# Optimization experiments

Hardware: AMD Instinct MI355X
Metric: run time of the kernel (lower is better)

Reference implementation:

```python
import jax, jax.numpy as jnp
import numpy as np

N = 100000
D_FEAT = 256
HID = 128
EMB = 64
FANOUT = 16


def setup_inputs() -> dict:
    key = jax.random.key(0)
    k = jax.random.split(key, 7)
    s = 0.05
    features = jax.random.normal(k[0], (N, D_FEAT), dtype=jnp.float32)
    W1 = jax.random.normal(k[1], (HID, 2 * D_FEAT), dtype=jnp.float32) * s
    W2 = jax.random.normal(k[2], (HID, 2 * HID), dtype=jnp.float32) * s
    W3 = jax.random.normal(k[3], (HID, 2 * HID), dtype=jnp.float32) * s
    W4 = jax.random.normal(k[4], (EMB, 2 * HID), dtype=jnp.float32) * s
    nodes = jnp.arange(N, dtype=jnp.int32)
    neigh = jax.random.randint(k[5], (N, FANOUT), 0, N, dtype=jnp.int32)
    return {"features": features, "W1": W1, "W2": W2, "W3": W3, "W4": W4,
            "nodes": nodes, "neigh": neigh}


def _sage_layer(h, neigh, W):
    # MeanAggregator: mean of sampled neighbor features  [N, d]
    neigh_mean = jnp.mean(h[neigh], axis=1)
    # Encoder (gcn=False): relu(W @ cat([self, neigh_mean]).T) -> [N, out]
    combined = jnp.concatenate([h, neigh_mean], axis=1)  # [N, 2d]
    return jax.nn.relu(combined @ W.T)


def reference(features, W1, W2, W3, W4, nodes, neigh):
    h1 = _sage_layer(features, neigh, W1)  # [N, HID]
    h2 = _sage_layer(h1, neigh, W2)        # [N, HID]
    h3 = _sage_layer(h2, neigh, W3)        # [N, HID]
    h4 = _sage_layer(h3, neigh, W4)        # [N, EMB]
    # GraphEmbeddingModule.forward returns gSAGE4(n).t() -> [len(n), EMB]
    return h4[nodes]
```

## Files before the change

### kernel.cpp

```cpp
#include <hip/hip_runtime.h>
#include <hip/hip_bf16.h>


constexpr int N_NODES = 100000;
constexpr int FANOUT  = 16;

typedef __attribute__((ext_vector_type(8))) short short8;
typedef __attribute__((ext_vector_type(4))) float f32x4;

__device__ inline unsigned short bf16_rne(float f) {
    unsigned u = __float_as_uint(f);
    return (unsigned short)((u + 0x7fffu + ((u >> 16) & 1u)) >> 16);
}
__device__ inline float bf16_tof(unsigned short s) {
    return __uint_as_float(((unsigned)s) << 16);
}

__global__ __launch_bounds__(256)
void prep_Bsw(const float* __restrict__ W, unsigned short* __restrict__ Bhi,
              unsigned short* __restrict__ Blo, int D_IN, int D_OUT)
{
    int i = blockIdx.x * 256 + threadIdx.x;
    int total = 2 * D_OUT * D_IN;
    if (i >= total) return;
    int K = D_IN, C = 2 * D_OUT;
    int c = i / K, k = i % K;
    float v = (c < D_OUT) ? W[(size_t)c * (2 * K) + k]
                          : W[(size_t)(c - D_OUT) * (2 * K) + K + k];
    int tc = c >> 4, mlc = c & 15;
    int tk = k >> 5, qk = (k >> 3) & 3, e = k & 7;
    size_t off = ((size_t)(tk * (C / 16) + tc) * 64 + qk * 16 + mlc) * 8 + e;
    unsigned short hi = bf16_rne(v);
    Bhi[off] = hi;
    Blo[off] = bf16_rne(v - bf16_tof(hi));
}

__global__ __launch_bounds__(256, 6)
void gemm1(const float* __restrict__ hf,
           const unsigned short* __restrict__ Bhi,
           const unsigned short* __restrict__ Blo,
           float* __restrict__ gs, unsigned short* __restrict__ gn, int N)
{
    constexpr int K = 256, DO = 128, LDA = 40;
    __shared__ unsigned short Ah[32 * LDA], Al[32 * LDA];

    const int tid  = threadIdx.x;
    const int wave = tid >> 6;
    const int lane = tid & 63;
    const int ml   = lane & 15;
    const int quad = lane >> 4;
    const int node0 = blockIdx.x * 32;

    const int srow = tid >> 3;
    const int sc4  = tid & 7;
    int nd = node0 + srow; if (nd >= N) nd = N - 1;
    const float* pA = &hf[(size_t)nd * K + sc4 * 4];

    f32x4 acc[2][4];
    #pragma unroll
    for (int mi = 0; mi < 2; ++mi)
        #pragma unroll
        for (int ni = 0; ni < 4; ++ni)
            acc[mi][ni] = (f32x4){0.f, 0.f, 0.f, 0.f};

    float4 pf = *(const float4*)&pA[0];

    for (int k0 = 0; k0 < K; k0 += 32) {
        {
            float vv[4] = {pf.x, pf.y, pf.z, pf.w};
            unsigned short hi[4], lo[4];
            #pragma unroll
            for (int e = 0; e < 4; ++e) {
                hi[e] = bf16_rne(vv[e]);
                lo[e] = bf16_rne(vv[e] - bf16_tof(hi[e]));
            }
            *(uint2*)&Ah[srow * LDA + sc4 * 4] = *(const uint2*)hi;
            *(uint2*)&Al[srow * LDA + sc4 * 4] = *(const uint2*)lo;
        }
        if (k0 + 32 < K) pf = *(const float4*)&pA[k0 + 32];
        __syncthreads();

        short8 afh[2], afl[2];
        #pragma unroll
        for (int mi = 0; mi < 2; ++mi) {
            int r = mi * 16 + ml;
            afh[mi] = *(const short8*)&Ah[r * LDA + quad * 8];
            afl[mi] = *(const short8*)&Al[r * LDA + quad * 8];
        }
        const size_t bbase = (size_t)((k0 >> 5) * 16 + wave * 4) * 512 + (size_t)lane * 8;
        #pragma unroll
        for (int ni = 0; ni < 4; ++ni) {
            short8 bh = *(const short8*)&Bhi[bbase + ni * 512];
            short8 bl = *(const short8*)&Blo[bbase + ni * 512];
            #pragma unroll
            for (int mi = 0; mi < 2; ++mi) {
                acc[mi][ni] = __builtin_amdgcn_mfma_f32_16x16x32_bf16(afl[mi], bh, acc[mi][ni], 0, 0, 0);
                acc[mi][ni] = __builtin_amdgcn_mfma_f32_16x16x32_bf16(afh[mi], bl, acc[mi][ni], 0, 0, 0);
                acc[mi][ni] = __builtin_amdgcn_mfma_f32_16x16x32_bf16(afh[mi], bh, acc[mi][ni], 0, 0, 0);
            }
        }
        __syncthreads();
    }

    #pragma unroll
    for (int mi = 0; mi < 2; ++mi)
        #pragma unroll
        for (int r = 0; r < 4; ++r) {
            int node = node0 + mi * 16 + quad * 4 + r;
            if (node >= N) continue;
            #pragma unroll
            for (int ni = 0; ni < 4; ++ni) {
                int c = wave * 64 + ni * 16 + ml;
                float v = acc[mi][ni][r];
                if (c < DO) gs[(size_t)node * DO + c] = v;
                else        gn[(size_t)node * DO + (c - DO)] = bf16_rne(v);
            }
        }
}

template<int C>
__global__ __launch_bounds__(256, 8)
void fused_layer(const float* __restrict__ gs_in,
                 const unsigned short* __restrict__ gn_in,
                 const int* __restrict__ neigh,
                 const unsigned short* __restrict__ Bhi,
                 const unsigned short* __restrict__ Blo,
                 float* __restrict__ gs_out,
                 unsigned short* __restrict__ gn_out, int N)
{
    constexpr int K = 128, DO = C / 2, NI = C / 64;
    __shared__ unsigned short Afh[32 * 128], Afl[32 * 128];

    const int tid  = threadIdx.x;
    const int wave = tid >> 6;
    const int lane = tid & 63;
    const int ml   = lane & 15;
    const int quad = lane >> 4;
    const int node0 = blockIdx.x * 32;

    {
        const int row = tid >> 3;
        const int s   = tid & 7;
        const int c0  = 64 * (s >> 2) + 8 * (s & 3);
        const int c1  = c0 + 32;
        int nd = node0 + row; if (nd >= N) nd = N - 1;
        const int4* nb4 = (const int4*)(neigh + (size_t)nd * FANOUT);
        int4 q0 = nb4[0], q1 = nb4[1], q2 = nb4[2], q3 = nb4[3];
        int ids[FANOUT] = {q0.x, q0.y, q0.z, q0.w, q1.x, q1.y, q1.z, q1.w,
                           q2.x, q2.y, q2.z, q2.w, q3.x, q3.y, q3.z, q3.w};
        float acc[16];
        #pragma unroll
        for (int c = 0; c < 16; ++c) acc[c] = 0.f;
        #pragma unroll
        for (int j = 0; j < FANOUT; ++j) {
            const uint4* src = (const uint4*)&gn_in[(size_t)ids[j] * 128];
            uint4 qa = src[c0 >> 3];
            uint4 qb = src[c1 >> 3];
            acc[0]  += __uint_as_float(qa.x << 16);
            acc[1]  += __uint_as_float(qa.x & 0xffff0000u);
            acc[2]  += __uint_as_float(qa.y << 16);
            acc[3]  += __uint_as_float(qa.y & 0xffff0000u);
            acc[4]  += __uint_as_float(qa.z << 16);
            acc[5]  += __uint_as_float(qa.z & 0xffff0000u);
            acc[6]  += __uint_as_float(qa.w << 16);
            acc[7]  += __uint_as_float(qa.w & 0xffff0000u);
            acc[8]  += __uint_as_float(qb.x << 16);
            acc[9]  += __uint_as_float(qb.x & 0xffff0000u);
            acc[10] += __uint_as_float(qb.y << 16);
            acc[11] += __uint_as_float(qb.y & 0xffff0000u);
            acc[12] += __uint_as_float(qb.z << 16);
            acc[13] += __uint_as_float(qb.z & 0xffff0000u);
            acc[14] += __uint_as_float(qb.w << 16);
            acc[15] += __uint_as_float(qb.w & 0xffff0000u);
        }
        const float inv = 1.0f / (float)FANOUT;
        const float* gsp = &gs_in[(size_t)nd * 128];
        #pragma unroll
        for (int cc = 0; cc < 2; ++cc) {
            const int ch = cc ? c1 : c0;
            float4 g0 = *(const float4*)&gsp[ch];
            float4 g1 = *(const float4*)&gsp[ch + 4];
            float sv[8] = {g0.x, g0.y, g0.z, g0.w, g1.x, g1.y, g1.z, g1.w};
            alignas(16) unsigned short th[8], tl[8];
            #pragma unroll
            for (int e = 0; e < 8; ++e) {
                float h = fmaxf(fmaf(acc[cc * 8 + e], inv, sv[e]), 0.f);
                unsigned short hi = bf16_rne(h);
                th[e] = hi;
                tl[e] = bf16_rne(h - bf16_tof(hi));
            }
            int soff = (row * 128 + ch) ^ ((row & 7) << 3);
            *(uint4*)&Afh[soff] = *(const uint4*)th;
            *(uint4*)&Afl[soff] = *(const uint4*)tl;
        }
    }
    __syncthreads();

    f32x4 acc[2][NI];
    #pragma unroll
    for (int mi = 0; mi < 2; ++mi)
        #pragma unroll
        for (int ni = 0; ni < NI; ++ni)
            acc[mi][ni] = (f32x4){0.f, 0.f, 0.f, 0.f};

    for (int k0 = 0; k0 < K; k0 += 32) {
        short8 afh[2], afl[2];
        #pragma unroll
        for (int mi = 0; mi < 2; ++mi) {
            int r = mi * 16 + ml;
            int soff = (r * 128 + k0 + quad * 8) ^ ((r & 7) << 3);
            afh[mi] = *(const short8*)&Afh[soff];
            afl[mi] = *(const short8*)&Afl[soff];
        }
        const size_t bbase = (size_t)((k0 >> 5) * (C / 16) + wave * NI) * 512 + (size_t)lane * 8;
        #pragma unroll
        for (int ni = 0; ni < NI; ++ni) {
            short8 bh = *(const short8*)&Bhi[bbase + ni * 512];
            short8 bl = *(const short8*)&Blo[bbase + ni * 512];
            #pragma unroll
            for (int mi = 0; mi < 2; ++mi) {
                acc[mi][ni] = __builtin_amdgcn_mfma_f32_16x16x32_bf16(afl[mi], bh, acc[mi][ni], 0, 0, 0);
                acc[mi][ni] = __builtin_amdgcn_mfma_f32_16x16x32_bf16(afh[mi], bl, acc[mi][ni], 0, 0, 0);
                acc[mi][ni] = __builtin_amdgcn_mfma_f32_16x16x32_bf16(afh[mi], bh, acc[mi][ni], 0, 0, 0);
            }
        }
    }

    #pragma unroll
    for (int mi = 0; mi < 2; ++mi)
        #pragma unroll
        for (int r = 0; r < 4; ++r) {
            int node = node0 + mi * 16 + quad * 4 + r;
            if (node >= N) continue;
            #pragma unroll
            for (int ni = 0; ni < NI; ++ni) {
                int c = wave * (16 * NI) + ni * 16 + ml;
                float v = acc[mi][ni][r];
                if (c < DO) gs_out[(size_t)node * DO + c] = v;
                else        gn_out[(size_t)node * DO + (c - DO)] = bf16_rne(v);
            }
        }
}

__global__ __launch_bounds__(256)
void agg_out(const float* __restrict__ gs4, const unsigned short* __restrict__ gn4,
             const int* __restrict__ neigh, const int* __restrict__ nodes,
             float* __restrict__ out, int N)
{
    const int i    = blockIdx.x * 32 + (threadIdx.x >> 3);
    const int lane = threadIdx.x & 7;
    if (i >= N) return;
    const int nd = nodes[i];
    const int4* nb4 = (const int4*)(neigh + (size_t)nd * FANOUT);
    int4 q0 = nb4[0], q1 = nb4[1], q2 = nb4[2], q3 = nb4[3];
    int ids[FANOUT] = {q0.x, q0.y, q0.z, q0.w, q1.x, q1.y, q1.z, q1.w,
                       q2.x, q2.y, q2.z, q2.w, q3.x, q3.y, q3.z, q3.w};
    float acc[8];
    #pragma unroll
    for (int c = 0; c < 8; ++c) acc[c] = 0.f;
    #pragma unroll
    for (int j = 0; j < FANOUT; ++j) {
        uint4 q = *(const uint4*)&gn4[(size_t)ids[j] * 64 + lane * 8];
        acc[0] += __uint_as_float(q.x << 16);
        acc[1] += __uint_as_float(q.x & 0xffff0000u);
        acc[2] += __uint_as_float(q.y << 16);
        acc[3] += __uint_as_float(q.y & 0xffff0000u);
        acc[4] += __uint_as_float(q.z << 16);
        acc[5] += __uint_as_float(q.z & 0xffff0000u);
        acc[6] += __uint_as_float(q.w << 16);
        acc[7] += __uint_as_float(q.w & 0xffff0000u);
    }
    const float inv = 1.0f / (float)FANOUT;
    const float* s = gs4 + (size_t)nd * 64 + lane * 8;
    float4 s0 = *(const float4*)&s[0];
    float4 s1 = *(const float4*)&s[4];
    float4 o0, o1;
    o0.x = fmaxf(fmaf(acc[0], inv, s0.x), 0.f);
    o0.y = fmaxf(fmaf(acc[1], inv, s0.y), 0.f);
    o0.z = fmaxf(fmaf(acc[2], inv, s0.z), 0.f);
    o0.w = fmaxf(fmaf(acc[3], inv, s0.w), 0.f);
    o1.x = fmaxf(fmaf(acc[4], inv, s1.x), 0.f);
    o1.y = fmaxf(fmaf(acc[5], inv, s1.y), 0.f);
    o1.z = fmaxf(fmaf(acc[6], inv, s1.z), 0.f);
    o1.w = fmaxf(fmaf(acc[7], inv, s1.w), 0.f);
    float* op = out + (size_t)i * 64 + lane * 8;
    *(float4*)&op[0] = o0;
    *(float4*)&op[4] = o1;
}

extern "C" void kernel_launch(void* const* d_in, const int* in_sizes, int n_in,
                              void* d_out, int out_size, void* d_ws, size_t ws_size,
                              hipStream_t stream)
{
    const float* features = (const float*)d_in[0];
    const float* W1       = (const float*)d_in[1];
    const float* W2       = (const float*)d_in[2];
    const float* W3       = (const float*)d_in[3];
    const float* W4       = (const float*)d_in[4];
    const int*   nodes    = (const int*)d_in[5];
    const int*   neigh    = (const int*)d_in[6];
    float*       out      = (float*)d_out;

    unsigned short* B1h = (unsigned short*)d_ws;
    unsigned short* B1l = B1h + 65536;
    unsigned short* B2h = B1l + 65536;
    unsigned short* B2l = B2h + 32768;
    unsigned short* B3h = B2l + 32768;
    unsigned short* B3l = B3h + 32768;
    unsigned short* B4h = B3l + 32768;
    unsigned short* B4l = B4h + 16384;
    float* gs = (float*)(B4l + 16384);
    unsigned short* gnA = (unsigned short*)(gs + (size_t)N_NODES * 128);
    unsigned short* gnB = gnA + (size_t)N_NODES * 128;
    float* gs4 = (float*)gnB;
    unsigned short* gn4 = gnB + (size_t)N_NODES * 128;

    prep_Bsw<<<(65536 + 255) / 256, 256, 0, stream>>>(W1, B1h, B1l, 256, 128);
    prep_Bsw<<<(32768 + 255) / 256, 256, 0, stream>>>(W2, B2h, B2l, 128, 128);
    prep_Bsw<<<(32768 + 255) / 256, 256, 0, stream>>>(W3, B3h, B3l, 128, 128);
    prep_Bsw<<<(16384 + 255) / 256, 256, 0, stream>>>(W4, B4h, B4l, 128, 64);

    const int grid32 = (N_NODES + 31) / 32;

    gemm1<<<grid32, 256, 0, stream>>>(features, B1h, B1l, gs, gnA, N_NODES);
    fused_layer<256><<<grid32, 256, 0, stream>>>(gs, gnA, neigh, B2h, B2l, gs, gnB, N_NODES);
    fused_layer<256><<<grid32, 256, 0, stream>>>(gs, gnB, neigh, B3h, B3l, gs, gnA, N_NODES);
    fused_layer<128><<<grid32, 256, 0, stream>>>(gs, gnA, neigh, B4h, B4l, gs4, gn4, N_NODES);
    agg_out<<<(N_NODES + 31) / 32, 256, 0, stream>>>(gs4, gn4, neigh, nodes, out, N_NODES);
}
```

Measured before the change: 484.3 us.

## Split aggregation into sliced-layout gather kernels separate from GEMMs

Stores the bf16 neighbour-projection buffers in a feature-sliced layout (8 slices of 16 columns, node-major within each slice). Aggregation moves out of the GEMM kernels into a standalone agg_act kernel, where each block handles one slice. The aim is to shrink the random-gather working set per pass so it fits in cache and improves L2 hit rate. The cost is extra kernel launches plus an additional read and write of the fp32 gs buffer for each layer.

```diff
diff --git a/kernel.cpp b/kernel.cpp
--- a/kernel.cpp
+++ b/kernel.cpp
@@ -39,7 +39,7 @@
 void gemm1(const float* __restrict__ hf,
            const unsigned short* __restrict__ Bhi,
            const unsigned short* __restrict__ Blo,
-           float* __restrict__ gs, unsigned short* __restrict__ gn, int N)
+           float* __restrict__ gs, unsigned short* __restrict__ gnS, int N)
 {
     constexpr int K = 256, DO = 128, LDA = 40;
     __shared__ unsigned short Ah[32 * LDA], Al[32 * LDA];
@@ -112,21 +112,72 @@
             for (int ni = 0; ni < 4; ++ni) {
                 int c = wave * 64 + ni * 16 + ml;
                 float v = acc[mi][ni][r];
-                if (c < DO) gs[(size_t)node * DO + c] = v;
-                else        gn[(size_t)node * DO + (c - DO)] = bf16_rne(v);
-            }
-        }
+                if (c < DO) gs[(size_t)node * 128 + c] = v;
+                else {
+                    int cs = c - DO;
+                    gnS[((size_t)(cs >> 4) * N + node) * 16 + (cs & 15)] = bf16_rne(v);
+                }
+            }
+        }
+}
+
+__global__ __launch_bounds__(256, 4)
+void agg_act(const unsigned short* __restrict__ gnS,
+             const int* __restrict__ neigh,
+             float* __restrict__ gs, int N)
+{
+    const int s = blockIdx.x & 7;
+    const int n = (blockIdx.x >> 3) * 256 + threadIdx.x;
+    if (n >= N) return;
+    const int4* nb4 = (const int4*)(neigh + (size_t)n * FANOUT);
+    int4 q0 = nb4[0], q1 = nb4[1], q2 = nb4[2], q3 = nb4[3];
+    int ids[FANOUT] = {q0.x, q0.y, q0.z, q0.w, q1.x, q1.y, q1.z, q1.w,
+                       q2.x, q2.y, q2.z, q2.w, q3.x, q3.y, q3.z, q3.w};
+    const unsigned short* base = gnS + (size_t)s * N * 16;
+    float acc[16];
+    #pragma unroll
+    for (int c = 0; c < 16; ++c) acc[c] = 0.f;
+    #pragma unroll
+    for (int j = 0; j < FANOUT; ++j) {
+        const uint4* p = (const uint4*)(base + (size_t)ids[j] * 16);
+        uint4 a = p[0], b = p[1];
+        acc[0]  += __uint_as_float(a.x << 16);
+        acc[1]  += __uint_as_float(a.x & 0xffff0000u);
+        acc[2]  += __uint_as_float(a.y << 16);
+        acc[3]  += __uint_as_float(a.y & 0xffff0000u);
+        acc[4]  += __uint_as_float(a.z << 16);
+        acc[5]  += __uint_as_float(a.z & 0xffff0000u);
+        acc[6]  += __uint_as_float(a.w << 16);
+        acc[7]  += __uint_as_float(a.w & 0xffff0000u);
+        acc[8]  += __uint_as_float(b.x << 16);
+        acc[9]  += __uint_as_float(b.x & 0xffff0000u);
+        acc[10] += __uint_as_float(b.y << 16);
+        acc[11] += __uint_as_float(b.y & 0xffff0000u);
+        acc[12] += __uint_as_float(b.z << 16);
+        acc[13] += __uint_as_float(b.z & 0xffff0000u);
+        acc[14] += __uint_as_float(b.w << 16);
+        acc[15] += __uint_as_float(b.w & 0xffff0000u);
+    }
+    const float inv = 1.0f / (float)FANOUT;
+    float* gp = gs + (size_t)n * 128 + s * 16;
+    #pragma unroll
+    for (int t = 0; t < 4; ++t) {
+        float4 g = *(const float4*)(gp + 4 * t);
+        g.x = fmaxf(fmaf(acc[4 * t + 0], inv, g.x), 0.f);
+        g.y = fmaxf(fmaf(acc[4 * t + 1], inv, g.y), 0.f);
+        g.z = fmaxf(fmaf(acc[4 * t + 2], inv, g.z), 0.f);
+        g.w = fmaxf(fmaf(acc[4 * t + 3], inv, g.w), 0.f);
+        *(float4*)(gp + 4 * t) = g;
+    }
 }
 
 template<int C>
-__global__ __launch_bounds__(256, 8)
-void fused_layer(const float* __restrict__ gs_in,
-                 const unsigned short* __restrict__ gn_in,
-                 const int* __restrict__ neigh,
-                 const unsigned short* __restrict__ Bhi,
-                 const unsigned short* __restrict__ Blo,
-                 float* __restrict__ gs_out,
-                 unsigned short* __restrict__ gn_out, int N)
+__global__ __launch_bounds__(256, 5)
+void gemm_mid(const float* __restrict__ hbuf,
+              const unsigned short* __restrict__ Bhi,
+              const unsigned short* __restrict__ Blo,
+              float* __restrict__ gs_out,
+              unsigned short* __restrict__ gnS_out, int N)
 {
     constexpr int K = 128, DO = C / 2, NI = C / 64;
     __shared__ unsigned short Afh[32 * 128], Afl[32 * 128];
@@ -139,57 +190,23 @@
     const int node0 = blockIdx.x * 32;
 
     {
-        const int row = tid >> 3;
-        const int s   = tid & 7;
-        const int c0  = 64 * (s >> 2) + 8 * (s & 3);
-        const int c1  = c0 + 32;
+        const int row  = tid >> 3;
+        const int sseg = tid & 7;
         int nd = node0 + row; if (nd >= N) nd = N - 1;
-        const int4* nb4 = (const int4*)(neigh + (size_t)nd * FANOUT);
-        int4 q0 = nb4[0], q1 = nb4[1], q2 = nb4[2], q3 = nb4[3];
-        int ids[FANOUT] = {q0.x, q0.y, q0.z, q0.w, q1.x, q1.y, q1.z, q1.w,
-                           q2.x, q2.y, q2.z, q2.w, q3.x, q3.y, q3.z, q3.w};
-        float acc[16];
-        #pragma unroll
-        for (int c = 0; c < 16; ++c) acc[c] = 0.f;
-        #pragma unroll
-        for (int j = 0; j < FANOUT; ++j) {
-            const uint4* src = (const uint4*)&gn_in[(size_t)ids[j] * 128];
-            uint4 qa = src[c0 >> 3];
-            uint4 qb = src[c1 >> 3];
-            acc[0]  += __uint_as_float(qa.x << 16);
-            acc[1]  += __uint_as_float(qa.x & 0xffff0000u);
-            acc[2]  += __uint_as_float(qa.y << 16);
-            acc[3]  += __uint_as_float(qa.y & 0xffff0000u);
-            acc[4]  += __uint_as_float(qa.z << 16);
-            acc[5]  += __uint_as_float(qa.z & 0xffff0000u);
-            acc[6]  += __uint_as_float(qa.w << 16);
-            acc[7]  += __uint_as_float(qa.w & 0xffff0000u);
-            acc[8]  += __uint_as_float(qb.x << 16);
-            acc[9]  += __uint_as_float(qb.x & 0xffff0000u);
-            acc[10] += __uint_as_float(qb.y << 16);
-            acc[11] += __uint_as_float(qb.y & 0xffff0000u);
-            acc[12] += __uint_as_float(qb.z << 16);
-            acc[13] += __uint_as_float(qb.z & 0xffff0000u);
-            acc[14] += __uint_as_float(qb.w << 16);
-            acc[15] += __uint_as_float(qb.w & 0xffff0000u);
-        }
-        const float inv = 1.0f / (float)FANOUT;
-        const float* gsp = &gs_in[(size_t)nd * 128];
+        const float* hp = &hbuf[(size_t)nd * 128 + sseg * 16];
         #pragma unroll
         for (int cc = 0; cc < 2; ++cc) {
-            const int ch = cc ? c1 : c0;
-            float4 g0 = *(const float4*)&gsp[ch];
-            float4 g1 = *(const float4*)&gsp[ch + 4];
-            float sv[8] = {g0.x, g0.y, g0.z, g0.w, g1.x, g1.y, g1.z, g1.w};
+            float4 v0 = *(const float4*)(hp + 8 * cc);
+            float4 v1 = *(const float4*)(hp + 8 * cc + 4);
+            float sv[8] = {v0.x, v0.y, v0.z, v0.w, v1.x, v1.y, v1.z, v1.w};
             alignas(16) unsigned short th[8], tl[8];
             #pragma unroll
             for (int e = 0; e < 8; ++e) {
-                float h = fmaxf(fmaf(acc[cc * 8 + e], inv, sv[e]), 0.f);
-                unsigned short hi = bf16_rne(h);
+                unsigned short hi = bf16_rne(sv[e]);
                 th[e] = hi;
-                tl[e] = bf16_rne(h - bf16_tof(hi));
-            }
-            int soff = (row * 128 + ch) ^ ((row & 7) << 3);
+                tl[e] = bf16_rne(sv[e] - bf16_tof(hi));
+            }
+            int soff = (row * 128 + sseg * 16 + 8 * cc) ^ ((row & 7) << 3);
             *(uint4*)&Afh[soff] = *(const uint4*)th;
             *(uint4*)&Afl[soff] = *(const uint4*)tl;
         }
@@ -236,31 +253,39 @@
             for (int ni = 0; ni < NI; ++ni) {
                 int c = wave * (16 * NI) + ni * 16 + ml;
                 float v = acc[mi][ni][r];
-                if (c < DO) gs_out[(size_t)node * DO + c] = v;
-                else        gn_out[(size_t)node * DO + (c - DO)] = bf16_rne(v);
-            }
-        }
-}
-
-__global__ __launch_bounds__(256)
-void agg_out(const float* __restrict__ gs4, const unsigned short* __restrict__ gn4,
-             const int* __restrict__ neigh, const int* __restrict__ nodes,
-             float* __restrict__ out, int N)
-{
-    const int i    = blockIdx.x * 32 + (threadIdx.x >> 3);
-    const int lane = threadIdx.x & 7;
-    if (i >= N) return;
-    const int nd = nodes[i];
+                if (c < DO) gs_out[(size_t)node * 128 + c] = v;
+                else {
+                    int cs = c - DO;
+                    if (C == 256)
+                        gnS_out[((size_t)(cs >> 4) * N + node) * 16 + (cs & 15)] = bf16_rne(v);
+                    else
+                        gnS_out[((size_t)(cs >> 3) * N + node) * 8 + (cs & 7)] = bf16_rne(v);
+                }
+            }
+        }
+}
+
+__global__ __launch_bounds__(256, 4)
+void agg_out_s(const float* __restrict__ gs,
+               const unsigned short* __restrict__ gn4S,
+               const int* __restrict__ neigh, const int* __restrict__ nodes,
+               float* __restrict__ out, int N)
+{
+    const int s = blockIdx.x & 7;
+    const int n = (blockIdx.x >> 3) * 256 + threadIdx.x;
+    if (n >= N) return;
+    const int nd = nodes[n];
     const int4* nb4 = (const int4*)(neigh + (size_t)nd * FANOUT);
     int4 q0 = nb4[0], q1 = nb4[1], q2 = nb4[2], q3 = nb4[3];
     int ids[FANOUT] = {q0.x, q0.y, q0.z, q0.w, q1.x, q1.y, q1.z, q1.w,
                        q2.x, q2.y, q2.z, q2.w, q3.x, q3.y, q3.z, q3.w};
+    const unsigned short* base = gn4S + (size_t)s * N * 8;
     float acc[8];
     #pragma unroll
     for (int c = 0; c < 8; ++c) acc[c] = 0.f;
     #pragma unroll
     for (int j = 0; j < FANOUT; ++j) {
-        uint4 q = *(const uint4*)&gn4[(size_t)ids[j] * 64 + lane * 8];
+        uint4 q = *(const uint4*)(base + (size_t)ids[j] * 8);
         acc[0] += __uint_as_float(q.x << 16);
         acc[1] += __uint_as_float(q.x & 0xffff0000u);
         acc[2] += __uint_as_float(q.y << 16);
@@ -271,21 +296,21 @@
         acc[7] += __uint_as_float(q.w & 0xffff0000u);
     }
     const float inv = 1.0f / (float)FANOUT;
-    const float* s = gs4 + (size_t)nd * 64 + lane * 8;
-    float4 s0 = *(const float4*)&s[0];
-    float4 s1 = *(const float4*)&s[4];
+    const float* gp = gs + (size_t)nd * 128 + s * 8;
+    float4 g0 = *(const float4*)(gp + 0);
+    float4 g1 = *(const float4*)(gp + 4);
     float4 o0, o1;
-    o0.x = fmaxf(fmaf(acc[0], inv, s0.x), 0.f);
-    o0.y = fmaxf(fmaf(acc[1], inv, s0.y), 0.f);
-    o0.z = fmaxf(fmaf(acc[2], inv, s0.z), 0.f);
-    o0.w = fmaxf(fmaf(acc[3], inv, s0.w), 0.f);
-    o1.x = fmaxf(fmaf(acc[4], inv, s1.x), 0.f);
-    o1.y = fmaxf(fmaf(acc[5], inv, s1.y), 0.f);
-    o1.z = fmaxf(fmaf(acc[6], inv, s1.z), 0.f);
-    o1.w = fmaxf(fmaf(acc[7], inv, s1.w), 0.f);
-    float* op = out + (size_t)i * 64 + lane * 8;
-    *(float4*)&op[0] = o0;
-    *(float4*)&op[4] = o1;
+    o0.x = fmaxf(fmaf(acc[0], inv, g0.x), 0.f);
+    o0.y = fmaxf(fmaf(acc[1], inv, g0.y), 0.f);
+    o0.z = fmaxf(fmaf(acc[2], inv, g0.z), 0.f);
+    o0.w = fmaxf(fmaf(acc[3], inv, g0.w), 0.f);
+    o1.x = fmaxf(fmaf(acc[4], inv, g1.x), 0.f);
+    o1.y = fmaxf(fmaf(acc[5], inv, g1.y), 0.f);
+    o1.z = fmaxf(fmaf(acc[6], inv, g1.z), 0.f);
+    o1.w = fmaxf(fmaf(acc[7], inv, g1.w), 0.f);
+    float* op = out + (size_t)n * 64 + s * 8;
+    *(float4*)(op + 0) = o0;
+    *(float4*)(op + 4) = o1;
 }
 
 extern "C" void kernel_launch(void* const* d_in, const int* in_sizes, int n_in,
@@ -310,10 +335,9 @@
     unsigned short* B4h = B3l + 32768;
     unsigned short* B4l = B4h + 16384;
     float* gs = (float*)(B4l + 16384);
-    unsigned short* gnA = (unsigned short*)(gs + (size_t)N_NODES * 128);
-    unsigned short* gnB = gnA + (size_t)N_NODES * 128;
-    float* gs4 = (float*)gnB;
-    unsigned short* gn4 = gnB + (size_t)N_NODES * 128;
+    unsigned short* gnSA = (unsigned short*)(gs + (size_t)N_NODES * 128);
+    unsigned short* gnSB = gnSA + (size_t)N_NODES * 128;
+    unsigned short* gn4S = gnSB;
 
     prep_Bsw<<<(65536 + 255) / 256, 256, 0, stream>>>(W1, B1h, B1l, 256, 128);
     prep_Bsw<<<(32768 + 255) / 256, 256, 0, stream>>>(W2, B2h, B2l, 128, 128);
@@ -321,10 +345,14 @@
     prep_Bsw<<<(16384 + 255) / 256, 256, 0, stream>>>(W4, B4h, B4l, 128, 64);
 
     const int grid32 = (N_NODES + 31) / 32;
-
-    gemm1<<<grid32, 256, 0, stream>>>(features, B1h, B1l, gs, gnA, N_NODES);
-    fused_layer<256><<<grid32, 256, 0, stream>>>(gs, gnA, neigh, B2h, B2l, gs, gnB, N_NODES);
-    fused_layer<256><<<grid32, 256, 0, stream>>>(gs, gnB, neigh, B3h, B3l, gs, gnA, N_NODES);
-    fused_layer<128><<<grid32, 256, 0, stream>>>(gs, gnA, neigh, B4h, B4l, gs4, gn4, N_NODES);
-    agg_out<<<(N_NODES + 31) / 32, 256, 0, stream>>>(gs4, gn4, neigh, nodes, out, N_NODES);
-}
+    const int gridA  = ((N_NODES + 255) / 256) * 8;
+
+    gemm1<<<grid32, 256, 0, stream>>>(features, B1h, B1l, gs, gnSA, N_NODES);
+    agg_act<<<gridA, 256, 0, stream>>>(gnSA, neigh, gs, N_NODES);
+    gemm_mid<256><<<grid32, 256, 0, stream>>>(gs, B2h, B2l, gs, gnSB, N_NODES);
+    agg_act<<<gridA, 256, 0, stream>>>(gnSB, neigh, gs, N_NODES);
+    gemm_mid<256><<<grid32, 256, 0, stream>>>(gs, B3h, B3l, gs, gnSA, N_NODES);
+    agg_act<<<gridA, 256, 0, stream>>>(gnSA, neigh, gs, N_NODES);
+    gemm_mid<128><<<grid32, 256, 0, stream>>>(gs, B4h, B4l, gs, gn4S, N_NODES);
+    agg_out_s<<<gridA, 256, 0, stream>>>(gs, gn4S, neigh, nodes, out, N_NODES);
+}
```

After: 736.4 us. +52.1%, slower.
